# Performance work log

Hardware: AMD Instinct MI355X
Metric: run time of the kernel (lower is better)

## Reference

```python
import jax, jax.numpy as jnp
import numpy as np

B, H, S, DK, DV = 2, 16, 2048, 64, 64


def setup_inputs() -> dict:
    key = jax.random.key(0)
    kq, kk, kv = jax.random.split(key, 3)
    queries = jax.random.normal(kq, (B, H, S, DK), dtype=jnp.float32)
    keys = jax.random.normal(kk, (B, H, S, DK), dtype=jnp.float32)
    values = jax.random.normal(kv, (B, H, S, DV), dtype=jnp.float32)
    # causal boolean mask, broadcastable over batch and heads
    mask = jnp.tril(jnp.ones((S, S), dtype=bool))[None, None, :, :]
    return {"queries": queries, "keys": keys, "values": values, "d_k": DK, "mask": mask}


def reference(queries, keys, values, d_k, mask):
    scale = 1.0 / jnp.sqrt(jnp.float32(d_k))
    # scores: [B, H, S, S]
    scores = jnp.einsum("bhqd,bhkd->bhqk", queries, keys) * scale
    mask_f = mask.astype(jnp.float32)
    scores = scores + (-1e9) * (1.0 - mask_f)
    weights = jax.nn.softmax(scores, axis=-1)
    # second mask step from the original: min(|mask|, |weights|)
    weights = jnp.minimum(jnp.abs(mask_f), jnp.abs(weights))
    return jnp.einsum("bhqk,bhkd->bhqd", weights, values)
```

## Files before the change

kernel.cpp:

```cpp
#include <hip/hip_runtime.h>
#include <hip/hip_bf16.h>

#define B_ 2
#define H_ 16
#define S_ 2048
#define D_ 64

typedef __attribute__((ext_vector_type(8))) short bf16x8;
typedef __attribute__((ext_vector_type(8))) unsigned short u16x8;
typedef __attribute__((ext_vector_type(2))) unsigned int u32x2;
typedef __attribute__((ext_vector_type(4))) float f32x4;
typedef unsigned short ushort_t;

#define SCALE 0.18033688011112042f

__device__ __forceinline__ unsigned short f2bf(float x) {
  unsigned int u = __builtin_bit_cast(unsigned int, x);
  unsigned int r = (u + 0x7FFFu + ((u >> 16) & 1u)) >> 16;
  return (unsigned short)r;
}

__device__ __forceinline__ unsigned int cvt_pk_bf16(float lo, float hi) {
  unsigned int r;
  asm("v_cvt_pk_bf16_f32 %0, %1, %2" : "=v"(r) : "v"(lo), "v"(hi));
  return r;
}

#define GLL16(gp, lp)                                                          \
  __builtin_amdgcn_global_load_lds(                                            \
      (const __attribute__((address_space(1))) unsigned int*)(gp),             \
      (__attribute__((address_space(3))) unsigned int*)(lp), 16, 0, 0)

__global__ void prepack(const float* __restrict__ Kf, const float* __restrict__ Vf,
                        ushort_t* __restrict__ Kg, ushort_t* __restrict__ Vtg) {
  const int blk = blockIdx.x;
  const int tid = threadIdx.x;
  const int bh = blk >> 5, t = blk & 31;
  const float* srcK = Kf + ((size_t)bh * S_ + (size_t)t * 64) * D_;
  const float* srcV = Vf + ((size_t)bh * S_ + (size_t)t * 64) * D_;
  ushort_t* dK = Kg + (size_t)blk * 4096;
  ushort_t* dV = Vtg + (size_t)blk * 4096;
  for (int is = 0; is < 2; ++is) {
    const int e = is * 2048 + tid * 8;
    {
      const int kv = e >> 6, pos = (e >> 3) & 7, ch = pos ^ (kv & 7);
      const float* sp = srcK + kv * 64 + ch * 8;
      float4 a = *(const float4*)sp;
      float4 b = *(const float4*)(sp + 4);
      u16x8 w;
      w[0] = f2bf(a.x); w[1] = f2bf(a.y); w[2] = f2bf(a.z); w[3] = f2bf(a.w);
      w[4] = f2bf(b.x); w[5] = f2bf(b.y); w[6] = f2bf(b.z); w[7] = f2bf(b.w);
      *(u16x8*)(dK + e) = w;
    }
    {
      const int d0 = e >> 6, pos = (e >> 3) & 7, ch = pos ^ (d0 & 7);
      u16x8 w;
      for (int i = 0; i < 8; ++i) w[i] = f2bf(srcV[(size_t)(ch * 8 + i) * 64 + d0]);
      *(u16x8*)(dV + e) = w;
    }
  }
}

template <int PRE>
__launch_bounds__(256, 3)
__global__ void attn3(const float* __restrict__ Qf, const float* __restrict__ Kf,
                      const float* __restrict__ Vf, const ushort_t* __restrict__ Kg,
                      const ushort_t* __restrict__ Vtg, float* __restrict__ O) {
  const int bh = blockIdx.x;
  const int qt = 31 - blockIdx.y;
  const int tid = threadIdx.x;
  const int wave = tid >> 6, lane = tid & 63;
  const int col = lane & 15, g = lane >> 4;

  __shared__ __align__(16) ushort_t Kl[2][64][64];
  __shared__ __align__(16) ushort_t Vt[2][64][64];
  __shared__ __align__(16) ushort_t Pl[4][16][72];

  float* Oh = O + (size_t)bh * S_ * D_;

  const int qrow = qt * 64 + wave * 16 + col;
  bf16x8 qf[2];
  {
    const float* Qh = Qf + (size_t)bh * S_ * D_;
    for (int kk = 0; kk < 2; ++kk) {
      const float* p = Qh + (size_t)qrow * 64 + kk * 32 + g * 8;
      float4 a = *(const float4*)p;
      float4 b = *(const float4*)(p + 4);
      float v[8] = {a.x, a.y, a.z, a.w, b.x, b.y, b.z, b.w};
      bf16x8 w;
      for (int i = 0; i < 8; ++i) w[i] = (short)f2bf(v[i] * SCALE);
      qf[kk] = w;
    }
  }

  f32x4 acc[4] = {};
  float m_ = -INFINITY, l_ = 0.0f;

  const int ch0 = (g ^ (col & 7)) << 3;
  const int ch1 = ((4 | g) ^ (col & 7)) << 3;

  auto STAGE = [&](int t, int b) {
    if (PRE) {
      const ushort_t* kg = Kg + ((size_t)(bh * 32 + t)) * 4096;
      const ushort_t* vg = Vtg + ((size_t)(bh * 32 + t)) * 4096;
      GLL16(kg + tid * 8,        &Kl[b][0][0] + tid * 8);
      GLL16(kg + 2048 + tid * 8, &Kl[b][0][0] + 2048 + tid * 8);
      GLL16(vg + tid * 8,        &Vt[b][0][0] + tid * 8);
      GLL16(vg + 2048 + tid * 8, &Vt[b][0][0] + 2048 + tid * 8);
    } else {
      const float* Kh = Kf + (size_t)bh * S_ * D_;
      const float* Vh = Vf + (size_t)bh * S_ * D_;
      {
        const int kvr = tid >> 2;
        const int c0 = (tid & 3) << 4;
        const float* src = Kh + ((size_t)(t * 64 + kvr)) * 64 + c0;
        for (int jj = 0; jj < 2; ++jj) {
          float4 x = *(const float4*)(src + jj * 8);
          float4 y = *(const float4*)(src + jj * 8 + 4);
          u16x8 w;
          w[0] = f2bf(x.x); w[1] = f2bf(x.y); w[2] = f2bf(x.z); w[3] = f2bf(x.w);
          w[4] = f2bf(y.x); w[5] = f2bf(y.y); w[6] = f2bf(y.z); w[7] = f2bf(y.w);
          const int ch = (c0 >> 3) + jj;
          *(u16x8*)&Kl[b][kvr][(ch ^ (kvr & 7)) << 3] = w;
        }
      }
      {
        const int c = tid & 63;
        const int r0 = (tid >> 6) << 4;
        const float* src = Vh + ((size_t)(t * 64 + r0)) * 64 + c;
        for (int jj = 0; jj < 2; ++jj) {
          u16x8 w;
          for (int i = 0; i < 8; ++i) w[i] = f2bf(src[(size_t)(jj * 8 + i) * 64]);
          const int ch = (r0 >> 3) + jj;
          *(u16x8*)&Vt[b][c][(ch ^ (c & 7)) << 3] = w;
        }
      }
    }
  };

  auto COMPUTE = [&](int b, bool diag) {
    f32x4 s[4] = {{0,0,0,0},{0,0,0,0},{0,0,0,0},{0,0,0,0}};
    __builtin_amdgcn_s_setprio(1);
    for (int nt = 0; nt < 4; ++nt) {
      const ushort_t* row = &Kl[b][nt * 16 + col][0];
      const bf16x8 kf0 = *(const bf16x8*)(row + ch0);
      const bf16x8 kf1 = *(const bf16x8*)(row + ch1);
      s[nt] = __builtin_amdgcn_mfma_f32_16x16x32_bf16(kf0, qf[0], s[nt], 0, 0, 0);
      s[nt] = __builtin_amdgcn_mfma_f32_16x16x32_bf16(kf1, qf[1], s[nt], 0, 0, 0);
    }
    __builtin_amdgcn_s_setprio(0);
    if (diag) {
      for (int nt = 0; nt < 4; ++nt)
        for (int r = 0; r < 4; ++r)
          if (nt * 16 + 4 * g + r > wave * 16 + col) s[nt][r] = -INFINITY;
    }
    float pm = fmaxf(fmaxf(fmaxf(s[0][0], s[0][1]), fmaxf(s[0][2], s[0][3])),
                     fmaxf(fmaxf(s[1][0], s[1][1]), fmaxf(s[1][2], s[1][3])));
    pm = fmaxf(pm, fmaxf(fmaxf(fmaxf(s[2][0], s[2][1]), fmaxf(s[2][2], s[2][3])),
                         fmaxf(fmaxf(s[3][0], s[3][1]), fmaxf(s[3][2], s[3][3]))));
    pm = fmaxf(pm, __shfl_xor(pm, 16));
    pm = fmaxf(pm, __shfl_xor(pm, 32));
    float fac = 1.0f;
    if (!__all(pm - m_ <= 8.0f)) {
      const float mn = fmaxf(m_, pm);
      fac = exp2f(m_ - mn);
      m_ = mn;
      for (int nt = 0; nt < 4; ++nt) acc[nt] *= fac;
    }
    float sum = 0.0f;
    for (int nt = 0; nt < 4; ++nt)
      for (int r = 0; r < 4; ++r) {
        const float p = exp2f(s[nt][r] - m_);
        s[nt][r] = p;
        sum += p;
      }
    sum += __shfl_xor(sum, 16);
    sum += __shfl_xor(sum, 32);
    l_ = l_ * fac + sum;
    for (int nt = 0; nt < 4; ++nt) {
      u32x2 w;
      w[0] = cvt_pk_bf16(s[nt][0], s[nt][1]);
      w[1] = cvt_pk_bf16(s[nt][2], s[nt][3]);
      *(u32x2*)&Pl[wave][col][nt * 16 + 4 * g] = w;
    }
    const bf16x8 pf0 = *(const bf16x8*)&Pl[wave][col][8 * g];
    const bf16x8 pf1 = *(const bf16x8*)&Pl[wave][col][32 + 8 * g];
    __builtin_amdgcn_s_setprio(1);
    for (int nt = 0; nt < 4; ++nt) {
      const ushort_t* row = &Vt[b][nt * 16 + col][0];
      const bf16x8 vf0 = *(const bf16x8*)(row + ch0);
      const bf16x8 vf1 = *(const bf16x8*)(row + ch1);
      acc[nt] = __builtin_amdgcn_mfma_f32_16x16x32_bf16(vf0, pf0, acc[nt], 0, 0, 0);
      acc[nt] = __builtin_amdgcn_mfma_f32_16x16x32_bf16(vf1, pf1, acc[nt], 0, 0, 0);
    }
    __builtin_amdgcn_s_setprio(0);
  };

  int cur = 0;
  STAGE(0, 0);
  __syncthreads();
  for (int t = 0; t <= qt; ++t) {
    if (t < qt) STAGE(t + 1, cur ^ 1);
    COMPUTE(cur, t == qt);
    __syncthreads();
    cur ^= 1;
  }

  const float inv = 1.0f / l_;
  float* dst = Oh + (size_t)qrow * 64;
  for (int nt = 0; nt < 4; ++nt) {
    f32x4 v = acc[nt];
    v *= inv;
    *(f32x4*)(dst + nt * 16 + 4 * g) = v;
  }
}

extern "C" void kernel_launch(void* const* d_in, const int* in_sizes, int n_in,
                              void* d_out, int out_size, void* d_ws, size_t ws_size,
                              hipStream_t stream) {
  const float* Q = (const float*)d_in[0];
  const float* K = (const float*)d_in[1];
  const float* V = (const float*)d_in[2];
  float* O = (float*)d_out;
  const size_t NE = (size_t)B_ * H_ * S_ * D_;
  if (ws_size >= 2 * NE * sizeof(ushort_t)) {
    ushort_t* kg = (ushort_t*)d_ws;
    prepack<<<1024, 256, 0, stream>>>(K, V, kg, kg + NE);
    attn3<1><<<dim3(32, 32), 256, 0, stream>>>(Q, K, V, kg, kg + NE, O);
  } else {
    attn3<0><<<dim3(32, 32), 256, 0, stream>>>(Q, K, V, nullptr, nullptr, O);
  }
}
```

Before: 61.05 us.

## Switch attention to 32x32x16 MFMA with register-resident P and two-wave blocks

Moves QK^T and PV from 16x16x32 to 32x32x16 bf16 MFMA, with each wave owning 32 query rows and blocks shrinking to 128 threads. K rows are permuted in the prepack (and the non-prepacked path) so the score accumulator layout matches the PV B-operand directly. This lets probabilities stay in registers instead of going through the shared-memory P buffer, and it removes one cross-lane shuffle per reduction. The trade-off is more accumulator registers per thread and fewer waves per block, which may lower latency hiding.

```diff
diff --git a/kernel.cpp b/kernel.cpp
--- a/kernel.cpp
+++ b/kernel.cpp
@@ -8,8 +8,9 @@
 
 typedef __attribute__((ext_vector_type(8))) short bf16x8;
 typedef __attribute__((ext_vector_type(8))) unsigned short u16x8;
-typedef __attribute__((ext_vector_type(2))) unsigned int u32x2;
-typedef __attribute__((ext_vector_type(4))) float f32x4;
+typedef __attribute__((ext_vector_type(16))) float f32x16;
+typedef __attribute__((ext_vector_type(4))) float f32x4v;
+typedef __attribute__((ext_vector_type(4))) unsigned int u32x4;
 typedef unsigned short ushort_t;
 
 #define SCALE 0.18033688011112042f
@@ -24,6 +25,21 @@
   unsigned int r;
   asm("v_cvt_pk_bf16_f32 %0, %1, %2" : "=v"(r) : "v"(lo), "v"(hi));
   return r;
+}
+
+__device__ __forceinline__ float vmax16(f32x16 v) {
+  float a = fmaxf(fmaxf(v[0], v[1]), fmaxf(v[2], v[3]));
+  float b = fmaxf(fmaxf(v[4], v[5]), fmaxf(v[6], v[7]));
+  float c = fmaxf(fmaxf(v[8], v[9]), fmaxf(v[10], v[11]));
+  float d = fmaxf(fmaxf(v[12], v[13]), fmaxf(v[14], v[15]));
+  return fmaxf(fmaxf(a, b), fmaxf(c, d));
+}
+__device__ __forceinline__ float vsum16(f32x16 v) {
+  float a = (v[0] + v[1]) + (v[2] + v[3]);
+  float b = (v[4] + v[5]) + (v[6] + v[7]);
+  float c = (v[8] + v[9]) + (v[10] + v[11]);
+  float d = (v[12] + v[13]) + (v[14] + v[15]);
+  return (a + b) + (c + d);
 }
 
 #define GLL16(gp, lp)                                                          \
@@ -43,8 +59,9 @@
   for (int is = 0; is < 2; ++is) {
     const int e = is * 2048 + tid * 8;
     {
-      const int kv = e >> 6, pos = (e >> 3) & 7, ch = pos ^ (kv & 7);
-      const float* sp = srcK + kv * 64 + ch * 8;
+      const int rl = e >> 6, pos = (e >> 3) & 7, ch = pos ^ (rl & 7);
+      const int kvs = (rl & 51) | ((rl & 4) << 1) | ((rl & 8) >> 1);
+      const float* sp = srcK + kvs * 64 + ch * 8;
       float4 a = *(const float4*)sp;
       float4 b = *(const float4*)(sp + 4);
       u16x8 w;
@@ -62,76 +79,78 @@
 }
 
 template <int PRE>
-__launch_bounds__(256, 3)
-__global__ void attn3(const float* __restrict__ Qf, const float* __restrict__ Kf,
+__launch_bounds__(128, 3)
+__global__ void attn5(const float* __restrict__ Qf, const float* __restrict__ Kf,
                       const float* __restrict__ Vf, const ushort_t* __restrict__ Kg,
                       const ushort_t* __restrict__ Vtg, float* __restrict__ O) {
   const int bh = blockIdx.x;
   const int qt = 31 - blockIdx.y;
   const int tid = threadIdx.x;
-  const int wave = tid >> 6, lane = tid & 63;
-  const int col = lane & 15, g = lane >> 4;
+  const int wq = tid >> 6, lane = tid & 63;
+  const int cq = lane & 31, hi = lane >> 5;
 
   __shared__ __align__(16) ushort_t Kl[2][64][64];
   __shared__ __align__(16) ushort_t Vt[2][64][64];
-  __shared__ __align__(16) ushort_t Pl[4][16][72];
-
-  float* Oh = O + (size_t)bh * S_ * D_;
-
-  const int qrow = qt * 64 + wave * 16 + col;
-  bf16x8 qf[2];
+
+  const int qrow = qt * 64 + wq * 32 + cq;
+
+  bf16x8 qf[4];
   {
-    const float* Qh = Qf + (size_t)bh * S_ * D_;
-    for (int kk = 0; kk < 2; ++kk) {
-      const float* p = Qh + (size_t)qrow * 64 + kk * 32 + g * 8;
-      float4 a = *(const float4*)p;
-      float4 b = *(const float4*)(p + 4);
-      float v[8] = {a.x, a.y, a.z, a.w, b.x, b.y, b.z, b.w};
+    const float* qp = Qf + (size_t)bh * S_ * D_ + (size_t)qrow * D_ + 8 * hi;
+    #pragma unroll
+    for (int ks = 0; ks < 4; ++ks) {
+      float4 a = *(const float4*)(qp + ks * 16);
+      float4 b = *(const float4*)(qp + ks * 16 + 4);
       bf16x8 w;
-      for (int i = 0; i < 8; ++i) w[i] = (short)f2bf(v[i] * SCALE);
-      qf[kk] = w;
-    }
-  }
-
-  f32x4 acc[4] = {};
+      w[0] = (short)f2bf(a.x * SCALE); w[1] = (short)f2bf(a.y * SCALE);
+      w[2] = (short)f2bf(a.z * SCALE); w[3] = (short)f2bf(a.w * SCALE);
+      w[4] = (short)f2bf(b.x * SCALE); w[5] = (short)f2bf(b.y * SCALE);
+      w[6] = (short)f2bf(b.z * SCALE); w[7] = (short)f2bf(b.w * SCALE);
+      qf[ks] = w;
+    }
+  }
+
+  f32x16 acc0 = {}, acc1 = {};
   float m_ = -INFINITY, l_ = 0.0f;
-
-  const int ch0 = (g ^ (col & 7)) << 3;
-  const int ch1 = ((4 | g) ^ (col & 7)) << 3;
+  const int chA = cq & 7;
 
   auto STAGE = [&](int t, int b) {
     if (PRE) {
       const ushort_t* kg = Kg + ((size_t)(bh * 32 + t)) * 4096;
       const ushort_t* vg = Vtg + ((size_t)(bh * 32 + t)) * 4096;
-      GLL16(kg + tid * 8,        &Kl[b][0][0] + tid * 8);
-      GLL16(kg + 2048 + tid * 8, &Kl[b][0][0] + 2048 + tid * 8);
-      GLL16(vg + tid * 8,        &Vt[b][0][0] + tid * 8);
-      GLL16(vg + 2048 + tid * 8, &Vt[b][0][0] + 2048 + tid * 8);
+      ushort_t* kl = &Kl[b][0][0];
+      ushort_t* vl = &Vt[b][0][0];
+      #pragma unroll
+      for (int j = 0; j < 4; ++j) {
+        GLL16(kg + j * 1024 + tid * 8, kl + j * 1024 + tid * 8);
+        GLL16(vg + j * 1024 + tid * 8, vl + j * 1024 + tid * 8);
+      }
     } else {
       const float* Kh = Kf + (size_t)bh * S_ * D_;
       const float* Vh = Vf + (size_t)bh * S_ * D_;
       {
-        const int kvr = tid >> 2;
-        const int c0 = (tid & 3) << 4;
-        const float* src = Kh + ((size_t)(t * 64 + kvr)) * 64 + c0;
-        for (int jj = 0; jj < 2; ++jj) {
+        const int rl = tid >> 1, h = tid & 1;
+        const int kvs = (rl & 51) | ((rl & 4) << 1) | ((rl & 8) >> 1);
+        const float* src = Kh + ((size_t)(t * 64 + kvs)) * 64 + h * 32;
+        #pragma unroll
+        for (int jj = 0; jj < 4; ++jj) {
           float4 x = *(const float4*)(src + jj * 8);
           float4 y = *(const float4*)(src + jj * 8 + 4);
           u16x8 w;
           w[0] = f2bf(x.x); w[1] = f2bf(x.y); w[2] = f2bf(x.z); w[3] = f2bf(x.w);
           w[4] = f2bf(y.x); w[5] = f2bf(y.y); w[6] = f2bf(y.z); w[7] = f2bf(y.w);
-          const int ch = (c0 >> 3) + jj;
-          *(u16x8*)&Kl[b][kvr][(ch ^ (kvr & 7)) << 3] = w;
+          const int ch = h * 4 + jj;
+          *(u16x8*)&Kl[b][rl][(ch ^ (rl & 7)) << 3] = w;
         }
       }
       {
-        const int c = tid & 63;
-        const int r0 = (tid >> 6) << 4;
-        const float* src = Vh + ((size_t)(t * 64 + r0)) * 64 + c;
-        for (int jj = 0; jj < 2; ++jj) {
+        const int c = tid & 63, rh = tid >> 6;
+        const float* sv = Vh + ((size_t)t * 64) * 64 + c;
+        #pragma unroll
+        for (int jj = 0; jj < 4; ++jj) {
+          const int ch = rh * 4 + jj;
           u16x8 w;
-          for (int i = 0; i < 8; ++i) w[i] = f2bf(src[(size_t)(jj * 8 + i) * 64]);
-          const int ch = (r0 >> 3) + jj;
+          for (int i = 0; i < 8; ++i) w[i] = f2bf(sv[(size_t)(ch * 8 + i) * 64]);
           *(u16x8*)&Vt[b][c][(ch ^ (c & 7)) << 3] = w;
         }
       }
@@ -139,60 +158,69 @@
   };
 
   auto COMPUTE = [&](int b, bool diag) {
-    f32x4 s[4] = {{0,0,0,0},{0,0,0,0},{0,0,0,0},{0,0,0,0}};
+    f32x16 s0 = {}, s1 = {};
     __builtin_amdgcn_s_setprio(1);
-    for (int nt = 0; nt < 4; ++nt) {
-      const ushort_t* row = &Kl[b][nt * 16 + col][0];
-      const bf16x8 kf0 = *(const bf16x8*)(row + ch0);
-      const bf16x8 kf1 = *(const bf16x8*)(row + ch1);
-      s[nt] = __builtin_amdgcn_mfma_f32_16x16x32_bf16(kf0, qf[0], s[nt], 0, 0, 0);
-      s[nt] = __builtin_amdgcn_mfma_f32_16x16x32_bf16(kf1, qf[1], s[nt], 0, 0, 0);
+    #pragma unroll
+    for (int ks = 0; ks < 4; ++ks) {
+      const int co = (((ks << 1) | hi) ^ chA) << 3;
+      const bf16x8 k0 = *(const bf16x8*)&Kl[b][cq][co];
+      const bf16x8 k1 = *(const bf16x8*)&Kl[b][32 + cq][co];
+      s0 = __builtin_amdgcn_mfma_f32_32x32x16_bf16(k0, qf[ks], s0, 0, 0, 0);
+      s1 = __builtin_amdgcn_mfma_f32_32x32x16_bf16(k1, qf[ks], s1, 0, 0, 0);
     }
     __builtin_amdgcn_s_setprio(0);
+
     if (diag) {
-      for (int nt = 0; nt < 4; ++nt)
-        for (int r = 0; r < 4; ++r)
-          if (nt * 16 + 4 * g + r > wave * 16 + col) s[nt][r] = -INFINITY;
-    }
-    float pm = fmaxf(fmaxf(fmaxf(s[0][0], s[0][1]), fmaxf(s[0][2], s[0][3])),
-                     fmaxf(fmaxf(s[1][0], s[1][1]), fmaxf(s[1][2], s[1][3])));
-    pm = fmaxf(pm, fmaxf(fmaxf(fmaxf(s[2][0], s[2][1]), fmaxf(s[2][2], s[2][3])),
-                         fmaxf(fmaxf(s[3][0], s[3][1]), fmaxf(s[3][2], s[3][3]))));
-    pm = fmaxf(pm, __shfl_xor(pm, 16));
+      const int qloc = wq * 32 + cq;
+      #pragma unroll
+      for (int r = 0; r < 16; ++r) {
+        const int tau = 16 * (r >> 3) + 4 * ((r >> 2) & 1) + (r & 3) + 8 * hi;
+        if (tau > qloc) s0[r] = -INFINITY;
+        if (32 + tau > qloc) s1[r] = -INFINITY;
+      }
+    }
+
+    float pm = fmaxf(vmax16(s0), vmax16(s1));
     pm = fmaxf(pm, __shfl_xor(pm, 32));
     float fac = 1.0f;
     if (!__all(pm - m_ <= 8.0f)) {
       const float mn = fmaxf(m_, pm);
       fac = exp2f(m_ - mn);
       m_ = mn;
-      for (int nt = 0; nt < 4; ++nt) acc[nt] *= fac;
-    }
-    float sum = 0.0f;
-    for (int nt = 0; nt < 4; ++nt)
-      for (int r = 0; r < 4; ++r) {
-        const float p = exp2f(s[nt][r] - m_);
-        s[nt][r] = p;
-        sum += p;
-      }
-    sum += __shfl_xor(sum, 16);
+      #pragma unroll
+      for (int r = 0; r < 16; ++r) { acc0[r] *= fac; acc1[r] *= fac; }
+    }
+    #pragma unroll
+    for (int r = 0; r < 16; ++r) {
+      s0[r] = exp2f(s0[r] - m_);
+      s1[r] = exp2f(s1[r] - m_);
+    }
+    float sum = vsum16(s0) + vsum16(s1);
     sum += __shfl_xor(sum, 32);
     l_ = l_ * fac + sum;
-    for (int nt = 0; nt < 4; ++nt) {
-      u32x2 w;
-      w[0] = cvt_pk_bf16(s[nt][0], s[nt][1]);
-      w[1] = cvt_pk_bf16(s[nt][2], s[nt][3]);
-      *(u32x2*)&Pl[wave][col][nt * 16 + 4 * g] = w;
-    }
-    const bf16x8 pf0 = *(const bf16x8*)&Pl[wave][col][8 * g];
-    const bf16x8 pf1 = *(const bf16x8*)&Pl[wave][col][32 + 8 * g];
+
+    unsigned W0[8], W1[8];
+    #pragma unroll
+    for (int j = 0; j < 8; ++j) {
+      W0[j] = cvt_pk_bf16(s0[2 * j], s0[2 * j + 1]);
+      W1[j] = cvt_pk_bf16(s1[2 * j], s1[2 * j + 1]);
+    }
+
     __builtin_amdgcn_s_setprio(1);
-    for (int nt = 0; nt < 4; ++nt) {
-      const ushort_t* row = &Vt[b][nt * 16 + col][0];
-      const bf16x8 vf0 = *(const bf16x8*)(row + ch0);
-      const bf16x8 vf1 = *(const bf16x8*)(row + ch1);
-      acc[nt] = __builtin_amdgcn_mfma_f32_16x16x32_bf16(vf0, pf0, acc[nt], 0, 0, 0);
-      acc[nt] = __builtin_amdgcn_mfma_f32_16x16x32_bf16(vf1, pf1, acc[nt], 0, 0, 0);
-    }
+#define PVSTEP(ks, Wm)                                                         \
+    {                                                                          \
+      u32x4 t4;                                                                \
+      t4[0] = Wm[4 * ((ks) & 1) + 0]; t4[1] = Wm[4 * ((ks) & 1) + 1];          \
+      t4[2] = Wm[4 * ((ks) & 1) + 2]; t4[3] = Wm[4 * ((ks) & 1) + 3];          \
+      const bf16x8 pf = __builtin_bit_cast(bf16x8, t4);                        \
+      const int co = ((((ks) << 1) | hi) ^ chA) << 3;                          \
+      const bf16x8 v0 = *(const bf16x8*)&Vt[b][cq][co];                        \
+      const bf16x8 v1 = *(const bf16x8*)&Vt[b][32 + cq][co];                   \
+      acc0 = __builtin_amdgcn_mfma_f32_32x32x16_bf16(v0, pf, acc0, 0, 0, 0);   \
+      acc1 = __builtin_amdgcn_mfma_f32_32x32x16_bf16(v1, pf, acc1, 0, 0, 0);   \
+    }
+    PVSTEP(0, W0) PVSTEP(1, W0) PVSTEP(2, W1) PVSTEP(3, W1)
+#undef PVSTEP
     __builtin_amdgcn_s_setprio(0);
   };
 
@@ -207,11 +235,17 @@
   }
 
   const float inv = 1.0f / l_;
-  float* dst = Oh + (size_t)qrow * 64;
-  for (int nt = 0; nt < 4; ++nt) {
-    f32x4 v = acc[nt];
-    v *= inv;
-    *(f32x4*)(dst + nt * 16 + 4 * g) = v;
+  float* dst = O + (size_t)bh * S_ * D_ + (size_t)qrow * D_;
+  #pragma unroll
+  for (int q2 = 0; q2 < 4; ++q2) {
+    f32x4v v0, v1;
+    #pragma unroll
+    for (int e = 0; e < 4; ++e) {
+      v0[e] = acc0[4 * q2 + e] * inv;
+      v1[e] = acc1[4 * q2 + e] * inv;
+    }
+    *(f32x4v*)(dst + 8 * q2 + 4 * hi) = v0;
+    *(f32x4v*)(dst + 32 + 8 * q2 + 4 * hi) = v1;
   }
 }
 
@@ -226,8 +260,8 @@
   if (ws_size >= 2 * NE * sizeof(ushort_t)) {
     ushort_t* kg = (ushort_t*)d_ws;
     prepack<<<1024, 256, 0, stream>>>(K, V, kg, kg + NE);
-    attn3<1><<<dim3(32, 32), 256, 0, stream>>>(Q, K, V, kg, kg + NE, O);
+    attn5<1><<<dim3(32, 32), 128, 0, stream>>>(Q, K, V, kg, kg + NE, O);
   } else {
-    attn3<0><<<dim3(32, 32), 256, 0, stream>>>(Q, K, V, nullptr, nullptr, O);
-  }
-}
+    attn5<0><<<dim3(32, 32), 128, 0, stream>>>(Q, K, V, nullptr, nullptr, O);
+  }
+}
```

After: 71.90 us. 1.18x slower.

## Permute K rows so P stays in registers, dropping LDS round-trip

Applied to the files above, without the earlier changes.

Applies a row permutation (sigma_row) to K when packing it into LDS/workspace. The QK^T MFMA output layout then matches the B-operand layout the PV MFMA expects, so probabilities are packed straight from registers into bf16 fragments. This removes the per-tile shared-memory store and reload of P along with its LDS allocation, and the causal mask indices are adjusted for the permutation. Launch bounds are raised to 4 blocks per SM to use the freed LDS, which risks register pressure.

```diff
diff --git a/kernel.cpp b/kernel.cpp
--- a/kernel.cpp
+++ b/kernel.cpp
@@ -8,7 +8,7 @@
 
 typedef __attribute__((ext_vector_type(8))) short bf16x8;
 typedef __attribute__((ext_vector_type(8))) unsigned short u16x8;
-typedef __attribute__((ext_vector_type(2))) unsigned int u32x2;
+typedef __attribute__((ext_vector_type(4))) unsigned int u32x4;
 typedef __attribute__((ext_vector_type(4))) float f32x4;
 typedef unsigned short ushort_t;
 
@@ -24,6 +24,10 @@
   unsigned int r;
   asm("v_cvt_pk_bf16_f32 %0, %1, %2" : "=v"(r) : "v"(lo), "v"(hi));
   return r;
+}
+
+__device__ __forceinline__ int sigma_row(int rl) {
+  return (rl & 0x23) | ((rl & 0x0C) << 1) | ((rl & 0x10) >> 2);
 }
 
 #define GLL16(gp, lp)                                                          \
@@ -43,8 +47,8 @@
   for (int is = 0; is < 2; ++is) {
     const int e = is * 2048 + tid * 8;
     {
-      const int kv = e >> 6, pos = (e >> 3) & 7, ch = pos ^ (kv & 7);
-      const float* sp = srcK + kv * 64 + ch * 8;
+      const int rl = e >> 6, pos = (e >> 3) & 7, ch = pos ^ (rl & 7);
+      const float* sp = srcK + sigma_row(rl) * 64 + ch * 8;
       float4 a = *(const float4*)sp;
       float4 b = *(const float4*)(sp + 4);
       u16x8 w;
@@ -62,8 +66,8 @@
 }
 
 template <int PRE>
-__launch_bounds__(256, 3)
-__global__ void attn3(const float* __restrict__ Qf, const float* __restrict__ Kf,
+__launch_bounds__(256, 4)
+__global__ void attn6(const float* __restrict__ Qf, const float* __restrict__ Kf,
                       const float* __restrict__ Vf, const ushort_t* __restrict__ Kg,
                       const ushort_t* __restrict__ Vtg, float* __restrict__ O) {
   const int bh = blockIdx.x;
@@ -74,7 +78,6 @@
 
   __shared__ __align__(16) ushort_t Kl[2][64][64];
   __shared__ __align__(16) ushort_t Vt[2][64][64];
-  __shared__ __align__(16) ushort_t Pl[4][16][72];
 
   float* Oh = O + (size_t)bh * S_ * D_;
 
@@ -111,9 +114,9 @@
       const float* Kh = Kf + (size_t)bh * S_ * D_;
       const float* Vh = Vf + (size_t)bh * S_ * D_;
       {
-        const int kvr = tid >> 2;
+        const int rl = tid >> 2;
         const int c0 = (tid & 3) << 4;
-        const float* src = Kh + ((size_t)(t * 64 + kvr)) * 64 + c0;
+        const float* src = Kh + ((size_t)(t * 64 + sigma_row(rl))) * 64 + c0;
         for (int jj = 0; jj < 2; ++jj) {
           float4 x = *(const float4*)(src + jj * 8);
           float4 y = *(const float4*)(src + jj * 8 + 4);
@@ -121,7 +124,7 @@
           w[0] = f2bf(x.x); w[1] = f2bf(x.y); w[2] = f2bf(x.z); w[3] = f2bf(x.w);
           w[4] = f2bf(y.x); w[5] = f2bf(y.y); w[6] = f2bf(y.z); w[7] = f2bf(y.w);
           const int ch = (c0 >> 3) + jj;
-          *(u16x8*)&Kl[b][kvr][(ch ^ (kvr & 7)) << 3] = w;
+          *(u16x8*)&Kl[b][rl][(ch ^ (rl & 7)) << 3] = w;
         }
       }
       {
@@ -150,9 +153,14 @@
     }
     __builtin_amdgcn_s_setprio(0);
     if (diag) {
-      for (int nt = 0; nt < 4; ++nt)
+      const int qloc = wave * 16 + col;
+      #pragma unroll
+      for (int nt = 0; nt < 4; ++nt) {
+        const int tau_base = 32 * (nt >> 1) + 4 * (nt & 1) + 8 * g;
+        #pragma unroll
         for (int r = 0; r < 4; ++r)
-          if (nt * 16 + 4 * g + r > wave * 16 + col) s[nt][r] = -INFINITY;
+          if (tau_base + r > qloc) s[nt][r] = -INFINITY;
+      }
     }
     float pm = fmaxf(fmaxf(fmaxf(s[0][0], s[0][1]), fmaxf(s[0][2], s[0][3])),
                      fmaxf(fmaxf(s[1][0], s[1][1]), fmaxf(s[1][2], s[1][3])));
@@ -177,14 +185,13 @@
     sum += __shfl_xor(sum, 16);
     sum += __shfl_xor(sum, 32);
     l_ = l_ * fac + sum;
-    for (int nt = 0; nt < 4; ++nt) {
-      u32x2 w;
-      w[0] = cvt_pk_bf16(s[nt][0], s[nt][1]);
-      w[1] = cvt_pk_bf16(s[nt][2], s[nt][3]);
-      *(u32x2*)&Pl[wave][col][nt * 16 + 4 * g] = w;
-    }
-    const bf16x8 pf0 = *(const bf16x8*)&Pl[wave][col][8 * g];
-    const bf16x8 pf1 = *(const bf16x8*)&Pl[wave][col][32 + 8 * g];
+    u32x4 t0, t1;
+    t0[0] = cvt_pk_bf16(s[0][0], s[0][1]); t0[1] = cvt_pk_bf16(s[0][2], s[0][3]);
+    t0[2] = cvt_pk_bf16(s[1][0], s[1][1]); t0[3] = cvt_pk_bf16(s[1][2], s[1][3]);
+    t1[0] = cvt_pk_bf16(s[2][0], s[2][1]); t1[1] = cvt_pk_bf16(s[2][2], s[2][3]);
+    t1[2] = cvt_pk_bf16(s[3][0], s[3][1]); t1[3] = cvt_pk_bf16(s[3][2], s[3][3]);
+    const bf16x8 pf0 = __builtin_bit_cast(bf16x8, t0);
+    const bf16x8 pf1 = __builtin_bit_cast(bf16x8, t1);
     __builtin_amdgcn_s_setprio(1);
     for (int nt = 0; nt < 4; ++nt) {
       const ushort_t* row = &Vt[b][nt * 16 + col][0];
@@ -226,8 +233,8 @@
   if (ws_size >= 2 * NE * sizeof(ushort_t)) {
     ushort_t* kg = (ushort_t*)d_ws;
     prepack<<<1024, 256, 0, stream>>>(K, V, kg, kg + NE);
-    attn3<1><<<dim3(32, 32), 256, 0, stream>>>(Q, K, V, kg, kg + NE, O);
+    attn6<1><<<dim3(32, 32), 256, 0, stream>>>(Q, K, V, kg, kg + NE, O);
   } else {
-    attn3<0><<<dim3(32, 32), 256, 0, stream>>>(Q, K, V, nullptr, nullptr, O);
-  }
-}
+    attn6<0><<<dim3(32, 32), 256, 0, stream>>>(Q, K, V, nullptr, nullptr, O);
+  }
+}
```

Measured after the change: 58.37 us. 1.05x faster.
